# Optimization experiments

Measured on AMD Instinct MI355X. Metric: run time of the kernel, lower is better.

The kernel has to match this reference:

```python
import jax, jax.numpy as jnp
import numpy as np

N_G, N_D, D = 50000, 50000, 64
R, L, NNZ, B = 32, 2, 1600000, 2048
TEMP, LAMBDA_1, LAMBDA_2, DROPOUT = 0.2, 0.2, 1e-7, 0.1


def setup_inputs() -> dict:
    key = jax.random.key(0)
    ks = jax.random.split(key, 14)
    uids = jax.random.randint(ks[0], (B,), 0, N_G)
    iids = jax.random.randint(ks[1], (B,), 0, N_D)
    pos = jax.random.randint(ks[2], (B,), 0, N_D)
    neg = jax.random.randint(ks[3], (B,), 0, N_D)
    E_g_0 = jax.random.normal(ks[4], (N_G, D), jnp.float32) * 0.01
    E_d_0 = jax.random.normal(ks[5], (N_D, D), jnp.float32) * 0.01
    rows = jax.random.randint(ks[6], (NNZ,), 0, N_G)
    cols = jax.random.randint(ks[7], (NNZ,), 0, N_D)
    vals = jax.random.uniform(ks[8], (NNZ,), jnp.float32)
    g_mul_s = jax.random.normal(ks[9], (N_G, R), jnp.float32) * 0.1
    v_mul_s = jax.random.normal(ks[10], (N_D, R), jnp.float32) * 0.1
    ut = jax.random.normal(ks[11], (R, N_G), jnp.float32) * (N_G ** -0.5)
    vt = jax.random.normal(ks[12], (R, N_D), jnp.float32) * (N_D ** -0.5)
    drop_u = jax.random.uniform(ks[13], (L, 2, NNZ), jnp.float32)
    return {"uids": uids, "iids": iids, "pos": pos, "neg": neg,
            "E_g_0": E_g_0, "E_d_0": E_d_0, "rows": rows, "cols": cols,
            "vals": vals, "g_mul_s": g_mul_s, "v_mul_s": v_mul_s,
            "ut": ut, "vt": vt, "drop_u": drop_u}


def reference(uids, iids, pos, neg, E_g_0, E_d_0, rows, cols, vals,
              g_mul_s, v_mul_s, ut, vt, drop_u):
    # sparse_dropout keep masks (independent per layer and per spmm call)
    keep = (drop_u > DROPOUT).astype(vals.dtype) / (1.0 - DROPOUT)  # [L,2,NNZ]
    E_g, E_d = E_g_0, E_d_0
    E_g_sum, E_d_sum = E_g_0, E_d_0
    G_g_sum, G_d_sum = E_g_0, E_d_0
    for layer in range(L):
        # Z_g = dropout(A) @ E_d ; Z_d = dropout(A).T @ E_g  (COO spmm)
        vg = vals * keep[layer, 0]
        Z_g = jax.ops.segment_sum(vg[:, None] * E_d[cols], rows, num_segments=N_G)
        vd = vals * keep[layer, 1]
        Z_d = jax.ops.segment_sum(vd[:, None] * E_g[rows], cols, num_segments=N_D)
        # low-rank SVD branch
        G_g = g_mul_s @ (vt @ E_d)  # [n_g, d]
        G_d = v_mul_s @ (ut @ E_g)  # [n_d, d]
        E_g, E_d = Z_g, Z_d
        E_g_sum = E_g_sum + E_g
        E_d_sum = E_d_sum + E_d
        G_g_sum = G_g_sum + G_g
        G_d_sum = G_d_sum + G_d
    # InfoNCE-style contrastive loss (exactly as torch: log(sum exp + eps))
    S_g = (G_g_sum[uids] @ E_g_sum.T) / TEMP  # [B, n_g]
    S_d = (G_d_sum[iids] @ E_d_sum.T) / TEMP  # [B, n_d]
    neg_score = jnp.log(jnp.exp(S_g).sum(1) + 1e-8).mean() \
              + jnp.log(jnp.exp(S_d).sum(1) + 1e-8).mean()
    pos_score = jnp.clip((G_g_sum[uids] * E_g_sum[uids]).sum(1) / TEMP, -5.0, 5.0).mean() \
              + jnp.clip((G_d_sum[iids] * E_d_sum[iids]).sum(1) / TEMP, -5.0, 5.0).mean()
    loss_s = -pos_score + neg_score
    # BPR loss
    g_emb = E_g_sum[uids]
    diff = (g_emb * E_d_sum[pos]).sum(-1) - (g_emb * E_d_sum[neg]).sum(-1)
    loss_r = -jnp.log(jax.nn.sigmoid(diff)).mean()
    # L2 reg over trainable embedding params
    loss_reg = LAMBDA_2 * (jnp.sum(E_g_0 ** 2) + jnp.sum(E_d_0 ** 2))
    loss = loss_r + LAMBDA_1 * loss_s + loss_reg
    return (loss, loss_r, LAMBDA_1 * loss_s)
```

## Files before the change

### kernel.cpp

```cpp
#include <hip/hip_runtime.h>
#include <hip/hip_bf16.h>
#include <math.h>

#define N_Gc 50000
#define N_Dc 50000
#define DIM 64
#define RNK 32
#define NNZc 1600000
#define BSZ 2048
#define KEEPV (1.0f/0.9f)
#define INVT 5.0f
#define NBK 782
#define CPAD 16
#define NSL 24
#define EPB 8000
#define MCH 256
#define MBLK 196

typedef __attribute__((ext_vector_type(8))) short bfrag;
typedef __attribute__((ext_vector_type(4))) float f32x4;

__device__ inline ushort f2bf(float f) {
  union { float f; unsigned int u; } v; v.f = f;
  unsigned int r = (v.u + 0x7fffu + ((v.u >> 16) & 1u)) >> 16;
  return (ushort)r;
}
__device__ inline float bf2f(ushort u) {
  union { unsigned int i; float f; } v; v.i = ((unsigned int)u) << 16;
  return v.f;
}

__global__ __launch_bounds__(256) void hist2_kernel(const int* __restrict__ rows, const int* __restrict__ cols,
                                                    int* __restrict__ bcnt_r, int* __restrict__ bcnt_c) {
  __shared__ int lh_r[NBK];
  __shared__ int lh_c[NBK];
  int t = threadIdx.x;
  for (int j = t; j < NBK; j += 256) { lh_r[j] = 0; lh_c[j] = 0; }
  __syncthreads();
  int e0 = blockIdx.x*EPB;
  for (int i = e0 + t; i < e0 + EPB; i += 256) {
    atomicAdd(&lh_r[rows[i] >> 6], 1);
    atomicAdd(&lh_c[cols[i] >> 6], 1);
  }
  __syncthreads();
  for (int j = t; j < NBK; j += 256) {
    int vr = lh_r[j]; if (vr) atomicAdd(&bcnt_r[j], vr);
    int vc = lh_c[j]; if (vc) atomicAdd(&bcnt_c[j], vc);
  }
}

__global__ __launch_bounds__(1024) void cscan_kernel(const int* __restrict__ bcnt_r, const int* __restrict__ bcnt_c,
                                                     int* __restrict__ gcur_r, int* __restrict__ gcur_c,
                                                     int* __restrict__ bptr_r, int* __restrict__ bptr_c) {
  const int* cnt = blockIdx.x ? bcnt_c : bcnt_r;
  int* gcur = blockIdx.x ? gcur_c : gcur_r;
  int* bptr = blockIdx.x ? bptr_c : bptr_r;
  __shared__ int wsum[16];
  int t = threadIdx.x, lane = t & 63, w = t >> 6;
  int v = (t < NBK) ? cnt[t] : 0;
  int x = v;
  #pragma unroll
  for (int o = 1; o < 64; o <<= 1) { int y = __shfl_up(x, o); if (lane >= o) x += y; }
  if (lane == 63) wsum[w] = x;
  __syncthreads();
  if (t < 16) {
    int s = wsum[t];
    #pragma unroll
    for (int o = 1; o < 16; o <<= 1) { int y = __shfl_up(s, o); if (t >= o) s += y; }
    wsum[t] = s;
  }
  __syncthreads();
  int ex = ((w == 0) ? 0 : wsum[w-1]) + (x - v);
  if (t < NBK) { gcur[t*CPAD] = ex; bptr[t] = ex; }
  if (t == 0) bptr[NBK] = wsum[15];
}

__global__ __launch_bounds__(256) void phaseA_kernel(const int* __restrict__ rows, const int* __restrict__ cols,
    const float* __restrict__ vals, const float* __restrict__ drop,
    int* __restrict__ gcur_r, int* __restrict__ gcur_c,
    uint2* __restrict__ stage_r, uint2* __restrict__ stage_c) {
  __shared__ int cnt_r[NBK], cnt_c[NBK];
  __shared__ int base_r[NBK], base_c[NBK];
  int t = threadIdx.x;
  for (int j = t; j < NBK; j += 256) { cnt_r[j] = 0; cnt_c[j] = 0; }
  __syncthreads();
  int e0 = blockIdx.x*EPB;
  for (int i = e0 + t; i < e0 + EPB; i += 256) {
    atomicAdd(&cnt_r[rows[i] >> 6], 1);
    atomicAdd(&cnt_c[cols[i] >> 6], 1);
  }
  __syncthreads();
  for (int j = t; j < NBK; j += 256) {
    int c = cnt_r[j]; base_r[j] = c ? atomicAdd(&gcur_r[j*CPAD], c) : 0; cnt_r[j] = 0;
    c = cnt_c[j];     base_c[j] = c ? atomicAdd(&gcur_c[j*CPAD], c) : 0; cnt_c[j] = 0;
  }
  __syncthreads();
  for (int i = e0 + t; i < e0 + EPB; i += 256) {
    int r = rows[i], c = cols[i];
    unsigned int vb = __float_as_uint(vals[i]);
    unsigned int dr0 = (drop[i] > 0.1f) ? (1u<<22) : 0u;
    unsigned int dc0 = (drop[(size_t)NNZc + i] > 0.1f) ? (1u<<22) : 0u;
    unsigned int dr1 = (drop[2*(size_t)NNZc + i] > 0.1f) ? (1u<<23) : 0u;
    unsigned int dc1 = (drop[3*(size_t)NNZc + i] > 0.1f) ? (1u<<23) : 0u;
    int br = r >> 6, bc = c >> 6;
    int p = base_r[br] + atomicAdd(&cnt_r[br], 1);
    stage_r[p] = make_uint2((unsigned int)c | ((unsigned int)(r & 63) << 16) | dr0 | dr1, vb);
    int q = base_c[bc] + atomicAdd(&cnt_c[bc], 1);
    stage_c[q] = make_uint2((unsigned int)r | ((unsigned int)(c & 63) << 16) | dc0 | dc1, vb);
  }
}

__global__ __launch_bounds__(256) void phaseB_kernel(const int* __restrict__ bptr, int* __restrict__ ptrout,
    const uint2* __restrict__ stage, ushort* __restrict__ fcol,
    float* __restrict__ fw0, float* __restrict__ fw1, int n) {
  __shared__ int cnt[64];
  __shared__ int pos[64];
  int t = threadIdx.x, b = blockIdx.x;
  int base_row = b*64;
  int base = bptr[b], endp = bptr[b+1];
  if (t < 64) cnt[t] = 0;
  __syncthreads();
  for (int k = base + t; k < endp; k += 256)
    atomicAdd(&cnt[(stage[k].x >> 16) & 63], 1);
  __syncthreads();
  if (t < 64) {
    int c = cnt[t], x = c;
    #pragma unroll
    for (int o = 1; o < 64; o <<= 1) { int y = __shfl_up(x, o); if (t >= o) x += y; }
    int excl = x - c;
    pos[t] = excl;
    int rr = base_row + t;
    if (rr <= n) ptrout[rr] = base + excl;
  }
  __syncthreads();
  for (int k = base + t; k < endp; k += 256) {
    uint2 rec = stage[k];
    int rel = (rec.x >> 16) & 63;
    int p = base + atomicAdd(&pos[rel], 1);
    float v = __uint_as_float(rec.y);
    fcol[p] = (ushort)(rec.x & 0xffffu);
    fw0[p] = (rec.x & (1u<<22)) ? v*KEEPV : 0.f;
    fw1[p] = (rec.x & (1u<<23)) ? v*KEEPV : 0.f;
  }
}

__global__ __launch_bounds__(256) void spmm_l0_kernel(const int* __restrict__ ptr,
    const ushort* __restrict__ fcol, const float* __restrict__ fw,
    const ushort* __restrict__ Eb, float* __restrict__ Z, ushort* __restrict__ Zb, int nrows) {
  int lane = threadIdx.x & 63;
  int row = blockIdx.x*4 + (threadIdx.x >> 6);
  if (row >= nrows) return;
  int k = ptr[row], end = ptr[row+1];
  float acc = 0.f;
  for (; k + 8 <= end; k += 8) {
    int cc[8]; float ww[8]; float gg[8];
    #pragma unroll
    for (int u = 0; u < 8; u++) { cc[u] = fcol[k+u]; ww[u] = fw[k+u]; }
    #pragma unroll
    for (int u = 0; u < 8; u++) gg[u] = bf2f(Eb[(size_t)cc[u]*DIM + lane]);
    #pragma unroll
    for (int u = 0; u < 8; u++) acc += ww[u]*gg[u];
  }
  for (; k < end; k++)
    acc += fw[k]*bf2f(Eb[(size_t)fcol[k]*DIM + lane]);
  size_t o = (size_t)row*DIM + lane;
  Z[o] = acc;
  Zb[o] = f2bf(acc);
}

__global__ __launch_bounds__(256) void spmm_l1_kernel(const int* __restrict__ ptr,
    const ushort* __restrict__ fcol, const float* __restrict__ fw,
    const ushort* __restrict__ Zb, const float* __restrict__ addA, const float* __restrict__ addB,
    ushort* __restrict__ Eout, int nrows) {
  int lane = threadIdx.x & 63;
  int row = blockIdx.x*4 + (threadIdx.x >> 6);
  if (row >= nrows) return;
  int k = ptr[row], end = ptr[row+1];
  float acc = 0.f;
  for (; k + 8 <= end; k += 8) {
    int cc[8]; float ww[8]; float gg[8];
    #pragma unroll
    for (int u = 0; u < 8; u++) { cc[u] = fcol[k+u]; ww[u] = fw[k+u]; }
    #pragma unroll
    for (int u = 0; u < 8; u++) gg[u] = bf2f(Zb[(size_t)cc[u]*DIM + lane]);
    #pragma unroll
    for (int u = 0; u < 8; u++) acc += ww[u]*gg[u];
  }
  for (; k < end; k++)
    acc += fw[k]*bf2f(Zb[(size_t)fcol[k]*DIM + lane]);
  size_t o = (size_t)row*DIM + lane;
  acc += addA[o] + addB[o];
  Eout[o] = f2bf(acc);
}

__global__ __launch_bounds__(256) void matred2_kernel(const float* __restrict__ vrow,
    const float* __restrict__ E0, const float* __restrict__ Z0,
    float* __restrict__ Mpart, int n) {
  __shared__ float vs[RNK*MCH];
  __shared__ float part[RNK*DIM];
  int t = threadIdx.x, lane = t & 63, w = t >> 6;
  int ci0 = blockIdx.x*MCH;
  int cnt = min(MCH, n - ci0);
  for (int idx = t; idx < RNK*DIM; idx += 256) part[idx] = 0.f;
  for (int idx = t; idx < RNK*MCH; idx += 256) {
    int r = idx >> 8, i = idx & (MCH-1);
    vs[idx] = (i < cnt) ? vrow[(size_t)r*n + ci0 + i] : 0.f;
  }
  __syncthreads();
  float acc[RNK];
  #pragma unroll
  for (int r = 0; r < RNK; r++) acc[r] = 0.f;
  int iw0 = w*64;
  for (int ii = 0; ii < 64; ii += 4) {
    int i = iw0 + ii;
    int gi = ci0 + i;
    float x0 = 0.f, x1 = 0.f, x2 = 0.f, x3 = 0.f;
    if (i + 3 < cnt) {
      x0 = E0[(size_t)(gi+0)*DIM + lane] + Z0[(size_t)(gi+0)*DIM + lane];
      x1 = E0[(size_t)(gi+1)*DIM + lane] + Z0[(size_t)(gi+1)*DIM + lane];
      x2 = E0[(size_t)(gi+2)*DIM + lane] + Z0[(size_t)(gi+2)*DIM + lane];
      x3 = E0[(size_t)(gi+3)*DIM + lane] + Z0[(size_t)(gi+3)*DIM + lane];
    } else {
      if (i+0 < cnt) x0 = E0[(size_t)(gi+0)*DIM + lane] + Z0[(size_t)(gi+0)*DIM + lane];
      if (i+1 < cnt) x1 = E0[(size_t)(gi+1)*DIM + lane] + Z0[(size_t)(gi+1)*DIM + lane];
      if (i+2 < cnt) x2 = E0[(size_t)(gi+2)*DIM + lane] + Z0[(size_t)(gi+2)*DIM + lane];
      if (i+3 < cnt) x3 = E0[(size_t)(gi+3)*DIM + lane] + Z0[(size_t)(gi+3)*DIM + lane];
    }
    #pragma unroll
    for (int r = 0; r < RNK; r++) {
      float4 v4 = *(const float4*)&vs[r*MCH + i];
      acc[r] += v4.x*x0 + v4.y*x1 + v4.z*x2 + v4.w*x3;
    }
  }
  #pragma unroll
  for (int r = 0; r < RNK; r++) atomicAdd(&part[r*DIM + lane], acc[r]);
  __syncthreads();
  float* dst = Mpart + (size_t)blockIdx.x*(RNK*DIM);
  for (int idx = t; idx < RNK*DIM; idx += 256) dst[idx] = part[idx];
}

__global__ __launch_bounds__(256) void mreduce_kernel(const float* __restrict__ Mpart,
    float* __restrict__ M, int nblk) {
  int idx = blockIdx.x*256 + threadIdx.x;
  if (idx < RNK*DIM) {
    float s = 0.f;
    for (int b = 0; b < nblk; b++) s += Mpart[(size_t)b*(RNK*DIM) + idx];
    M[idx] = s;
  }
}

__global__ __launch_bounds__(256) void gsmall_kernel(const int* __restrict__ ids,
    const float* __restrict__ E0, const float* __restrict__ mul, const float* __restrict__ M,
    float* __restrict__ out, ushort* __restrict__ outb) {
  __shared__ float Ms[RNK*DIM];
  int t = threadIdx.x;
  for (int i = t; i < RNK*DIM; i += 256) Ms[i] = M[i];
  __syncthreads();
  int b = blockIdx.x*4 + (t >> 6), lane = t & 63;
  int u = ids[b];
  float a = E0[(size_t)u*DIM + lane];
  #pragma unroll
  for (int r = 0; r < RNK; r++) a += mul[(size_t)u*RNK + r]*Ms[r*DIM + lane];
  out[(size_t)b*DIM + lane] = a;
  outb[(size_t)b*DIM + lane] = f2bf(a);
}

__global__ __launch_bounds__(256) void convsq_kernel(const float4* __restrict__ in,
    ushort4* __restrict__ out, int n4, float* __restrict__ acc) {
  __shared__ float ls[4];
  int t = threadIdx.x;
  int idx = blockIdx.x*256 + t;
  int stride = gridDim.x*256;
  float s = 0.f;
  for (int i = idx; i < n4; i += stride) {
    float4 v = in[i];
    ushort4 o;
    o.x = f2bf(v.x); o.y = f2bf(v.y); o.z = f2bf(v.z); o.w = f2bf(v.w);
    out[i] = o;
    s += v.x*v.x + v.y*v.y + v.z*v.z + v.w*v.w;
  }
  #pragma unroll
  for (int o = 32; o > 0; o >>= 1) s += __shfl_xor(s, o);
  if ((t & 63) == 0) ls[t >> 6] = s;
  __syncthreads();
  if (t == 0) atomicAdd(acc, ls[0] + ls[1] + ls[2] + ls[3]);
}

__global__ __launch_bounds__(256) void lse_mfma_kernel(const ushort* __restrict__ A,
    const ushort* __restrict__ X, int nj, float* __restrict__ sumexp) {
  __shared__ __align__(16) ushort Xs[64*68];
  int t = threadIdx.x, lane = t & 63, w = t >> 6;
  int bt = blockIdx.x & 31, js = blockIdx.x >> 5;
  int b0 = bt*64;
  int m = lane & 15, q = lane >> 4;
  const ushort* Arow = A + (size_t)(b0 + w*16 + m)*DIM + q*8;
  bfrag a0 = *(const bfrag*)(Arow);
  bfrag a1 = *(const bfrag*)(Arow + 32);
  float rs0 = 0.f, rs1 = 0.f, rs2 = 0.f, rs3 = 0.f;
  int njt = (nj + 63) >> 6;
  for (int jt = js; jt < njt; jt += NSL) {
    int j0 = jt << 6;
    __syncthreads();
    for (int c = t; c < 512; c += 256) {
      int r = c >> 3, k8 = (c & 7) << 3;
      int j = j0 + r;
      ushort4 v0 = {0,0,0,0}, v1 = {0,0,0,0};
      if (j < nj) {
        const ushort4* src = (const ushort4*)(X + (size_t)j*DIM + k8);
        v0 = src[0]; v1 = src[1];
      }
      *(ushort4*)&Xs[r*68 + k8]     = v0;
      *(ushort4*)&Xs[r*68 + k8 + 4] = v1;
    }
    __syncthreads();
    #pragma unroll
    for (int jq = 0; jq < 4; jq++) {
      int jr = jq*16 + m;
      union { bfrag f; uint2 u2[2]; } B0, B1;
      B0.u2[0] = *(const uint2*)&Xs[jr*68 + q*8];
      B0.u2[1] = *(const uint2*)&Xs[jr*68 + q*8 + 4];
      B1.u2[0] = *(const uint2*)&Xs[jr*68 + 32 + q*8];
      B1.u2[1] = *(const uint2*)&Xs[jr*68 + 32 + q*8 + 4];
      f32x4 acc = {0.f, 0.f, 0.f, 0.f};
      acc = __builtin_amdgcn_mfma_f32_16x16x32_bf16(a0, B0.f, acc, 0, 0, 0);
      acc = __builtin_amdgcn_mfma_f32_16x16x32_bf16(a1, B1.f, acc, 0, 0, 0);
      int jg = j0 + jr;
      if (jg < nj) {
        rs0 += __expf(acc[0]*INVT);
        rs1 += __expf(acc[1]*INVT);
        rs2 += __expf(acc[2]*INVT);
        rs3 += __expf(acc[3]*INVT);
      }
    }
  }
  #pragma unroll
  for (int o = 1; o < 16; o <<= 1) {
    rs0 += __shfl_xor(rs0, o);
    rs1 += __shfl_xor(rs1, o);
    rs2 += __shfl_xor(rs2, o);
    rs3 += __shfl_xor(rs3, o);
  }
  if (m == 0) {
    float* dst = &sumexp[b0 + w*16 + q*4];
    atomicAdd(&dst[0], rs0);
    atomicAdd(&dst[1], rs1);
    atomicAdd(&dst[2], rs2);
    atomicAdd(&dst[3], rs3);
  }
}

__global__ __launch_bounds__(256) void perb_kernel(const int* __restrict__ uids, const int* __restrict__ iids,
    const int* __restrict__ pos, const int* __restrict__ neg,
    const float* __restrict__ Ggu, const float* __restrict__ Gdi,
    const ushort* __restrict__ Egs_b, const ushort* __restrict__ Eds_b,
    const float* __restrict__ seg, const float* __restrict__ sed,
    float* __restrict__ accs) {
  __shared__ float lsum[3][4];
  int t = threadIdx.x, lane = t & 63, w = t >> 6;
  int b = blockIdx.x*4 + w;
  int u = uids[b], it = iids[b], p = pos[b], ng = neg[b];
  float egu = bf2f(Egs_b[(size_t)u*DIM + lane]);
  float d1 = Ggu[(size_t)b*DIM + lane]*egu;
  float d2 = Gdi[(size_t)b*DIM + lane]*bf2f(Eds_b[(size_t)it*DIM + lane]);
  float d3 = egu*bf2f(Eds_b[(size_t)p*DIM + lane]);
  float d4 = egu*bf2f(Eds_b[(size_t)ng*DIM + lane]);
  #pragma unroll
  for (int o = 32; o > 0; o >>= 1) {
    d1 += __shfl_xor(d1, o);
    d2 += __shfl_xor(d2, o);
    d3 += __shfl_xor(d3, o);
    d4 += __shfl_xor(d4, o);
  }
  if (lane == 0) {
    float pterm = fminf(fmaxf(d1*INVT, -5.f), 5.f) + fminf(fmaxf(d2*INVT, -5.f), 5.f);
    float diff = d3 - d4;
    lsum[0][w] = pterm;
    lsum[1][w] = log1pf(expf(-diff));
    lsum[2][w] = logf(seg[b] + 1e-8f) + logf(sed[b] + 1e-8f);
  }
  __syncthreads();
  if (t < 3) atomicAdd(&accs[t], lsum[t][0] + lsum[t][1] + lsum[t][2] + lsum[t][3]);
}

__global__ void final_kernel(const float* __restrict__ accs, float* __restrict__ out) {
  float posm = accs[0]*(1.f/BSZ);
  float lr   = accs[1]*(1.f/BSZ);
  float negm = accs[2]*(1.f/BSZ);
  float reg  = 1e-7f*accs[3];
  float l1ls = 0.2f*(negm - posm);
  out[0] = lr + l1ls + reg;
  out[1] = lr;
  out[2] = l1ls;
}

extern "C" void kernel_launch(void* const* d_in, const int* in_sizes, int n_in,
                              void* d_out, int out_size, void* d_ws, size_t ws_size,
                              hipStream_t stream) {
  (void)in_sizes; (void)n_in; (void)out_size;
  const int*   uids = (const int*)d_in[0];
  const int*   iids = (const int*)d_in[1];
  const int*   pos  = (const int*)d_in[2];
  const int*   neg  = (const int*)d_in[3];
  const float* Eg0  = (const float*)d_in[4];
  const float* Ed0  = (const float*)d_in[5];
  const int*   rows = (const int*)d_in[6];
  const int*   cols = (const int*)d_in[7];
  const float* vals = (const float*)d_in[8];
  const float* gms  = (const float*)d_in[9];
  const float* vms  = (const float*)d_in[10];
  const float* ut   = (const float*)d_in[11];
  const float* vt   = (const float*)d_in[12];
  const float* drop = (const float*)d_in[13];
  float* out = (float*)d_out;

  float* ws = (float*)d_ws;
  const size_t ED = (size_t)N_Gc*DIM;
  float* Zg0  = ws;
  float* Zd0  = Zg0 + ED;
  float* REG1 = Zd0 + ED;
  float* REG2 = REG1 + ED;
  int* ptr_r = (int*)(REG2 + ED);
  int* ptr_c = ptr_r + (N_Gc + 1);
  int* bcnt_r = ptr_c + (N_Dc + 1);
  int* bcnt_c = bcnt_r + NBK;
  int* bptr_r = bcnt_c + NBK;
  int* bptr_c = bptr_r + (NBK + 1);
  int* gcur_r = bptr_c + (NBK + 1);
  int* gcur_c = gcur_r + NBK*CPAD;
  ushort* fcol_r = (ushort*)(gcur_c + NBK*CPAD);
  float* fw_r0  = (float*)(fcol_r + NNZc);
  float* fw_r1  = fw_r0 + NNZc;
  ushort* fcol_c = (ushort*)(fw_r1 + NNZc);
  float* fw_c0  = (float*)(fcol_c + NNZc);
  float* fw_c1  = fw_c0 + NNZc;
  float* Ggu = fw_c1 + NNZc;
  float* Gdi = Ggu + (size_t)BSZ*DIM;
  ushort* Ggu_b = (ushort*)(Gdi + (size_t)BSZ*DIM);
  ushort* Gdi_b = Ggu_b + (size_t)BSZ*DIM;
  float* Mg  = (float*)(Gdi_b + (size_t)BSZ*DIM);
  float* Md  = Mg + RNK*DIM;
  float* seg = Md + RNK*DIM;
  float* sed = seg + BSZ;
  float* accs = sed + BSZ;
  float* MpG = accs + 16;
  float* MpD = MpG + (size_t)MBLK*RNK*DIM;

  uint2* stage_r = (uint2*)Zg0;
  uint2* stage_c = (uint2*)REG1;
  ushort* Eg0_b = (ushort*)REG1;
  ushort* Ed0_b = Eg0_b + ED;
  ushort* Egs_b = (ushort*)REG1;
  ushort* Eds_b = Egs_b + ED;
  ushort* Zg0_b = (ushort*)REG2;
  ushort* Zd0_b = Zg0_b + ED;

  size_t need = ((char*)(MpD + (size_t)MBLK*RNK*DIM)) - ((char*)d_ws);
  if (ws_size < need) return;

  hipMemsetAsync(bcnt_r, 0, sizeof(int)*(2*NBK), stream);
  hipMemsetAsync(Mg, 0, sizeof(float)*(2*RNK*DIM + 2*BSZ + 16), stream);

  hist2_kernel<<<NNZc/EPB, 256, 0, stream>>>(rows, cols, bcnt_r, bcnt_c);
  cscan_kernel<<<2, 1024, 0, stream>>>(bcnt_r, bcnt_c, gcur_r, gcur_c, bptr_r, bptr_c);
  phaseA_kernel<<<NNZc/EPB, 256, 0, stream>>>(rows, cols, vals, drop, gcur_r, gcur_c, stage_r, stage_c);
  phaseB_kernel<<<NBK, 256, 0, stream>>>(bptr_r, ptr_r, stage_r, fcol_r, fw_r0, fw_r1, N_Gc);
  phaseB_kernel<<<NBK, 256, 0, stream>>>(bptr_c, ptr_c, stage_c, fcol_c, fw_c0, fw_c1, N_Dc);

  int n4 = (int)(ED/4);
  convsq_kernel<<<1024, 256, 0, stream>>>((const float4*)Eg0, (ushort4*)Eg0_b, n4, accs + 3);
  convsq_kernel<<<1024, 256, 0, stream>>>((const float4*)Ed0, (ushort4*)Ed0_b, n4, accs + 3);

  int spmm_blocks = (N_Gc + 3)/4;
  spmm_l0_kernel<<<spmm_blocks, 256, 0, stream>>>(ptr_r, fcol_r, fw_r0, Ed0_b, Zg0, Zg0_b, N_Gc);
  spmm_l0_kernel<<<spmm_blocks, 256, 0, stream>>>(ptr_c, fcol_c, fw_c0, Eg0_b, Zd0, Zd0_b, N_Dc);
  spmm_l1_kernel<<<spmm_blocks, 256, 0, stream>>>(ptr_r, fcol_r, fw_r1, Zd0_b, Eg0, Zg0, Egs_b, N_Gc);
  spmm_l1_kernel<<<spmm_blocks, 256, 0, stream>>>(ptr_c, fcol_c, fw_c1, Zg0_b, Ed0, Zd0, Eds_b, N_Dc);

  matred2_kernel<<<MBLK, 256, 0, stream>>>(vt, Ed0, Zd0, MpG, N_Dc);
  matred2_kernel<<<MBLK, 256, 0, stream>>>(ut, Eg0, Zg0, MpD, N_Gc);
  mreduce_kernel<<<(RNK*DIM + 255)/256, 256, 0, stream>>>(MpG, Mg, MBLK);
  mreduce_kernel<<<(RNK*DIM + 255)/256, 256, 0, stream>>>(MpD, Md, MBLK);

  gsmall_kernel<<<BSZ/4, 256, 0, stream>>>(uids, Eg0, gms, Mg, Ggu, Ggu_b);
  gsmall_kernel<<<BSZ/4, 256, 0, stream>>>(iids, Ed0, vms, Md, Gdi, Gdi_b);

  lse_mfma_kernel<<<32*NSL, 256, 0, stream>>>(Ggu_b, Egs_b, N_Gc, seg);
  lse_mfma_kernel<<<32*NSL, 256, 0, stream>>>(Gdi_b, Eds_b, N_Dc, sed);

  perb_kernel<<<BSZ/4, 256, 0, stream>>>(uids, iids, pos, neg, Ggu, Gdi, Egs_b, Eds_b, seg, sed, accs);
  final_kernel<<<1, 1, 0, stream>>>(accs, out);
}
```

Measured before the change: 675.0 us.

## Replace atomic bucket allocation with per-block count matrix scan and wider buckets

The COO-to-CSR build now groups rows into 256-row buckets instead of 64-row buckets. Each block writes its local bucket histogram into a bucket-by-block count matrix. A single scan over that matrix gives every block a fixed write offset, replacing the global atomic cursor reservation in phaseA. This removes global atomics and the bcnt memset. In exchange the scan is a serial loop over about 39K entries, phaseB handles larger buckets with a 256-wide local scan, and the Mg/Md memset is dropped.

```diff
diff --git a/kernel.cpp b/kernel.cpp
--- a/kernel.cpp
+++ b/kernel.cpp
@@ -10,8 +10,8 @@
 #define BSZ 2048
 #define KEEPV (1.0f/0.9f)
 #define INVT 5.0f
-#define NBK 782
-#define CPAD 16
+#define NBK2 196
+#define NBLK 200
 #define NSL 24
 #define EPB 8000
 #define MCH 256
@@ -30,117 +30,126 @@
   return v.f;
 }
 
-__global__ __launch_bounds__(256) void hist2_kernel(const int* __restrict__ rows, const int* __restrict__ cols,
-                                                    int* __restrict__ bcnt_r, int* __restrict__ bcnt_c) {
-  __shared__ int lh_r[NBK];
-  __shared__ int lh_c[NBK];
-  int t = threadIdx.x;
-  for (int j = t; j < NBK; j += 256) { lh_r[j] = 0; lh_c[j] = 0; }
-  __syncthreads();
-  int e0 = blockIdx.x*EPB;
+__global__ __launch_bounds__(256) void hist3_kernel(const int* __restrict__ rows, const int* __restrict__ cols,
+                                                    int* __restrict__ cntR, int* __restrict__ cntC) {
+  __shared__ int lh_r[NBK2];
+  __shared__ int lh_c[NBK2];
+  int t = threadIdx.x, blk = blockIdx.x;
+  if (t < NBK2) { lh_r[t] = 0; lh_c[t] = 0; }
+  __syncthreads();
+  int e0 = blk*EPB;
   for (int i = e0 + t; i < e0 + EPB; i += 256) {
-    atomicAdd(&lh_r[rows[i] >> 6], 1);
-    atomicAdd(&lh_c[cols[i] >> 6], 1);
-  }
-  __syncthreads();
-  for (int j = t; j < NBK; j += 256) {
-    int vr = lh_r[j]; if (vr) atomicAdd(&bcnt_r[j], vr);
-    int vc = lh_c[j]; if (vc) atomicAdd(&bcnt_c[j], vc);
-  }
-}
-
-__global__ __launch_bounds__(1024) void cscan_kernel(const int* __restrict__ bcnt_r, const int* __restrict__ bcnt_c,
-                                                     int* __restrict__ gcur_r, int* __restrict__ gcur_c,
-                                                     int* __restrict__ bptr_r, int* __restrict__ bptr_c) {
-  const int* cnt = blockIdx.x ? bcnt_c : bcnt_r;
-  int* gcur = blockIdx.x ? gcur_c : gcur_r;
-  int* bptr = blockIdx.x ? bptr_c : bptr_r;
+    atomicAdd(&lh_r[rows[i] >> 8], 1);
+    atomicAdd(&lh_c[cols[i] >> 8], 1);
+  }
+  __syncthreads();
+  if (t < NBK2) {
+    cntR[t*NBLK + blk] = lh_r[t];
+    cntC[t*NBLK + blk] = lh_c[t];
+  }
+}
+
+__global__ __launch_bounds__(1024) void cscan2_kernel(const int* __restrict__ cntA, int* __restrict__ cbA, int* __restrict__ bpA,
+                                                      const int* __restrict__ cntB, int* __restrict__ cbB, int* __restrict__ bpB) {
+  const int n = NBK2*NBLK;
+  const int* cnt = blockIdx.x ? cntB : cntA;
+  int* cb = blockIdx.x ? cbB : cbA;
+  int* bp = blockIdx.x ? bpB : bpA;
   __shared__ int wsum[16];
   int t = threadIdx.x, lane = t & 63, w = t >> 6;
-  int v = (t < NBK) ? cnt[t] : 0;
-  int x = v;
-  #pragma unroll
-  for (int o = 1; o < 64; o <<= 1) { int y = __shfl_up(x, o); if (lane >= o) x += y; }
-  if (lane == 63) wsum[w] = x;
-  __syncthreads();
-  if (t < 16) {
-    int s = wsum[t];
-    #pragma unroll
-    for (int o = 1; o < 16; o <<= 1) { int y = __shfl_up(s, o); if (t >= o) s += y; }
-    wsum[t] = s;
-  }
-  __syncthreads();
-  int ex = ((w == 0) ? 0 : wsum[w-1]) + (x - v);
-  if (t < NBK) { gcur[t*CPAD] = ex; bptr[t] = ex; }
-  if (t == 0) bptr[NBK] = wsum[15];
-}
-
-__global__ __launch_bounds__(256) void phaseA_kernel(const int* __restrict__ rows, const int* __restrict__ cols,
+  int carry = 0;
+  for (int base = 0; base < n; base += 1024) {
+    int i = base + t;
+    int v = (i < n) ? cnt[i] : 0;
+    int x = v;
+    #pragma unroll
+    for (int o = 1; o < 64; o <<= 1) { int y = __shfl_up(x, o); if (lane >= o) x += y; }
+    if (lane == 63) wsum[w] = x;
+    __syncthreads();
+    if (t < 16) {
+      int s = wsum[t];
+      #pragma unroll
+      for (int o = 1; o < 16; o <<= 1) { int y = __shfl_up(s, o); if (t >= o) s += y; }
+      wsum[t] = s;
+    }
+    __syncthreads();
+    int wpre = (w == 0) ? 0 : wsum[w-1];
+    int total = wsum[15];
+    int ex = carry + wpre + (x - v);
+    if (i < n) {
+      cb[i] = ex;
+      if (i % NBLK == 0) bp[i/NBLK] = ex;
+    }
+    carry += total;
+    __syncthreads();
+  }
+  if (t == 0) bp[NBK2] = carry;
+}
+
+__global__ __launch_bounds__(256) void phaseA2_kernel(const int* __restrict__ rows, const int* __restrict__ cols,
     const float* __restrict__ vals, const float* __restrict__ drop,
-    int* __restrict__ gcur_r, int* __restrict__ gcur_c,
+    const int* __restrict__ cbR, const int* __restrict__ cbC,
     uint2* __restrict__ stage_r, uint2* __restrict__ stage_c) {
-  __shared__ int cnt_r[NBK], cnt_c[NBK];
-  __shared__ int base_r[NBK], base_c[NBK];
-  int t = threadIdx.x;
-  for (int j = t; j < NBK; j += 256) { cnt_r[j] = 0; cnt_c[j] = 0; }
-  __syncthreads();
-  int e0 = blockIdx.x*EPB;
-  for (int i = e0 + t; i < e0 + EPB; i += 256) {
-    atomicAdd(&cnt_r[rows[i] >> 6], 1);
-    atomicAdd(&cnt_c[cols[i] >> 6], 1);
-  }
-  __syncthreads();
-  for (int j = t; j < NBK; j += 256) {
-    int c = cnt_r[j]; base_r[j] = c ? atomicAdd(&gcur_r[j*CPAD], c) : 0; cnt_r[j] = 0;
-    c = cnt_c[j];     base_c[j] = c ? atomicAdd(&gcur_c[j*CPAD], c) : 0; cnt_c[j] = 0;
-  }
-  __syncthreads();
+  __shared__ int cnt_r[NBK2], cnt_c[NBK2];
+  __shared__ int base_r[NBK2], base_c[NBK2];
+  int t = threadIdx.x, blk = blockIdx.x;
+  if (t < NBK2) {
+    cnt_r[t] = 0; cnt_c[t] = 0;
+    base_r[t] = cbR[t*NBLK + blk];
+    base_c[t] = cbC[t*NBLK + blk];
+  }
+  __syncthreads();
+  int e0 = blk*EPB;
   for (int i = e0 + t; i < e0 + EPB; i += 256) {
     int r = rows[i], c = cols[i];
     unsigned int vb = __float_as_uint(vals[i]);
-    unsigned int dr0 = (drop[i] > 0.1f) ? (1u<<22) : 0u;
-    unsigned int dc0 = (drop[(size_t)NNZc + i] > 0.1f) ? (1u<<22) : 0u;
-    unsigned int dr1 = (drop[2*(size_t)NNZc + i] > 0.1f) ? (1u<<23) : 0u;
-    unsigned int dc1 = (drop[3*(size_t)NNZc + i] > 0.1f) ? (1u<<23) : 0u;
-    int br = r >> 6, bc = c >> 6;
+    unsigned int dr0 = (drop[i] > 0.1f) ? (1u<<24) : 0u;
+    unsigned int dc0 = (drop[(size_t)NNZc + i] > 0.1f) ? (1u<<24) : 0u;
+    unsigned int dr1 = (drop[2*(size_t)NNZc + i] > 0.1f) ? (1u<<25) : 0u;
+    unsigned int dc1 = (drop[3*(size_t)NNZc + i] > 0.1f) ? (1u<<25) : 0u;
+    int br = r >> 8, bc = c >> 8;
     int p = base_r[br] + atomicAdd(&cnt_r[br], 1);
-    stage_r[p] = make_uint2((unsigned int)c | ((unsigned int)(r & 63) << 16) | dr0 | dr1, vb);
+    stage_r[p] = make_uint2((unsigned int)c | ((unsigned int)(r & 255) << 16) | dr0 | dr1, vb);
     int q = base_c[bc] + atomicAdd(&cnt_c[bc], 1);
-    stage_c[q] = make_uint2((unsigned int)r | ((unsigned int)(c & 63) << 16) | dc0 | dc1, vb);
-  }
-}
-
-__global__ __launch_bounds__(256) void phaseB_kernel(const int* __restrict__ bptr, int* __restrict__ ptrout,
+    stage_c[q] = make_uint2((unsigned int)r | ((unsigned int)(c & 255) << 16) | dc0 | dc1, vb);
+  }
+}
+
+__global__ __launch_bounds__(256) void phaseB2_kernel(const int* __restrict__ bptr, int* __restrict__ ptrout,
     const uint2* __restrict__ stage, ushort* __restrict__ fcol,
     float* __restrict__ fw0, float* __restrict__ fw1, int n) {
-  __shared__ int cnt[64];
-  __shared__ int pos[64];
+  __shared__ int cnt[256];
+  __shared__ int pos[256];
+  __shared__ int woff[4];
   int t = threadIdx.x, b = blockIdx.x;
-  int base_row = b*64;
+  int base_row = b*256;
   int base = bptr[b], endp = bptr[b+1];
-  if (t < 64) cnt[t] = 0;
+  cnt[t] = 0;
   __syncthreads();
   for (int k = base + t; k < endp; k += 256)
-    atomicAdd(&cnt[(stage[k].x >> 16) & 63], 1);
-  __syncthreads();
-  if (t < 64) {
-    int c = cnt[t], x = c;
-    #pragma unroll
-    for (int o = 1; o < 64; o <<= 1) { int y = __shfl_up(x, o); if (t >= o) x += y; }
-    int excl = x - c;
-    pos[t] = excl;
-    int rr = base_row + t;
-    if (rr <= n) ptrout[rr] = base + excl;
-  }
+    atomicAdd(&cnt[(stage[k].x >> 16) & 255], 1);
+  __syncthreads();
+  int lane = t & 63, w = t >> 6;
+  int c = cnt[t], x = c;
+  #pragma unroll
+  for (int o = 1; o < 64; o <<= 1) { int y = __shfl_up(x, o); if (lane >= o) x += y; }
+  if (lane == 63) woff[w] = x;
+  __syncthreads();
+  if (t == 0) { woff[1] += woff[0]; woff[2] += woff[1]; woff[3] += woff[2]; }
+  __syncthreads();
+  int excl = ((w == 0) ? 0 : woff[w-1]) + (x - c);
+  pos[t] = excl;
+  int rr = base_row + t;
+  if (rr <= n) ptrout[rr] = base + excl;
   __syncthreads();
   for (int k = base + t; k < endp; k += 256) {
     uint2 rec = stage[k];
-    int rel = (rec.x >> 16) & 63;
+    int rel = (rec.x >> 16) & 255;
     int p = base + atomicAdd(&pos[rel], 1);
     float v = __uint_as_float(rec.y);
     fcol[p] = (ushort)(rec.x & 0xffffu);
-    fw0[p] = (rec.x & (1u<<22)) ? v*KEEPV : 0.f;
-    fw1[p] = (rec.x & (1u<<23)) ? v*KEEPV : 0.f;
+    fw0[p] = (rec.x & (1u<<24)) ? v*KEEPV : 0.f;
+    fw1[p] = (rec.x & (1u<<25)) ? v*KEEPV : 0.f;
   }
 }
 
@@ -421,13 +430,13 @@
   float* REG2 = REG1 + ED;
   int* ptr_r = (int*)(REG2 + ED);
   int* ptr_c = ptr_r + (N_Gc + 1);
-  int* bcnt_r = ptr_c + (N_Dc + 1);
-  int* bcnt_c = bcnt_r + NBK;
-  int* bptr_r = bcnt_c + NBK;
-  int* bptr_c = bptr_r + (NBK + 1);
-  int* gcur_r = bptr_c + (NBK + 1);
-  int* gcur_c = gcur_r + NBK*CPAD;
-  ushort* fcol_r = (ushort*)(gcur_c + NBK*CPAD);
+  int* bptr_r = ptr_c + (N_Dc + 1);
+  int* bptr_c = bptr_r + (NBK2 + 1);
+  int* cntR = bptr_c + (NBK2 + 1);
+  int* cntC = cntR + NBK2*NBLK;
+  int* cbR  = cntC + NBK2*NBLK;
+  int* cbC  = cbR + NBK2*NBLK;
+  ushort* fcol_r = (ushort*)(cbC + NBK2*NBLK);
   float* fw_r0  = (float*)(fcol_r + NNZc);
   float* fw_r1  = fw_r0 + NNZc;
   ushort* fcol_c = (ushort*)(fw_r1 + NNZc);
@@ -457,14 +466,13 @@
   size_t need = ((char*)(MpD + (size_t)MBLK*RNK*DIM)) - ((char*)d_ws);
   if (ws_size < need) return;
 
-  hipMemsetAsync(bcnt_r, 0, sizeof(int)*(2*NBK), stream);
-  hipMemsetAsync(Mg, 0, sizeof(float)*(2*RNK*DIM + 2*BSZ + 16), stream);
-
-  hist2_kernel<<<NNZc/EPB, 256, 0, stream>>>(rows, cols, bcnt_r, bcnt_c);
-  cscan_kernel<<<2, 1024, 0, stream>>>(bcnt_r, bcnt_c, gcur_r, gcur_c, bptr_r, bptr_c);
-  phaseA_kernel<<<NNZc/EPB, 256, 0, stream>>>(rows, cols, vals, drop, gcur_r, gcur_c, stage_r, stage_c);
-  phaseB_kernel<<<NBK, 256, 0, stream>>>(bptr_r, ptr_r, stage_r, fcol_r, fw_r0, fw_r1, N_Gc);
-  phaseB_kernel<<<NBK, 256, 0, stream>>>(bptr_c, ptr_c, stage_c, fcol_c, fw_c0, fw_c1, N_Dc);
+  hipMemsetAsync(seg, 0, sizeof(float)*(2*BSZ + 16), stream);
+
+  hist3_kernel<<<NBLK, 256, 0, stream>>>(rows, cols, cntR, cntC);
+  cscan2_kernel<<<2, 1024, 0, stream>>>(cntR, cbR, bptr_r, cntC, cbC, bptr_c);
+  phaseA2_kernel<<<NBLK, 256, 0, stream>>>(rows, cols, vals, drop, cbR, cbC, stage_r, stage_c);
+  phaseB2_kernel<<<NBK2, 256, 0, stream>>>(bptr_r, ptr_r, stage_r, fcol_r, fw_r0, fw_r1, N_Gc);
+  phaseB2_kernel<<<NBK2, 256, 0, stream>>>(bptr_c, ptr_c, stage_c, fcol_c, fw_c0, fw_c1, N_Dc);
 
   int n4 = (int)(ED/4);
   convsq_kernel<<<1024, 256, 0, stream>>>((const float4*)Eg0, (ushort4*)Eg0_b, n4, accs + 3);
```

Measured after the change: 687.2 us. About the same (+1.8%).
